# Kernel optimization log

Hardware: AMD Instinct MI355X
Metric: run time of the kernel (lower is better)

The kernel has to match this reference:

```python
import jax, jax.numpy as jnp
import numpy as np
import math

D_K = 1024
HEADS = 16
HEAD_DIM = 64

def setup_inputs() -> dict:
    key = jax.random.key(0)
    ks = jax.random.split(key, 9)
    B, S, E = 2, 2048, D_K
    sc = 0.02
    return {
        "x": jax.random.normal(ks[0], (B, S, E), dtype=jnp.float32),
        "mask": 1,
        "Wq": jax.random.normal(ks[1], (E, E), dtype=jnp.float32) * sc,
        "bq": jnp.zeros((E,), dtype=jnp.float32),
        "Wk": jax.random.normal(ks[2], (E, E), dtype=jnp.float32) * sc,
        "bk": jnp.zeros((E,), dtype=jnp.float32),
        "Wv": jax.random.normal(ks[3], (E, E), dtype=jnp.float32) * sc,
        "bv": jnp.zeros((E,), dtype=jnp.float32),
        "Wo": jax.random.normal(ks[4], (E, E), dtype=jnp.float32) * sc,
        "bo": jnp.zeros((E,), dtype=jnp.float32),
    }

def reference(x, mask, Wq, bq, Wk, bk, Wv, bv, Wo, bo):
    B, S, E = x.shape
    H, Dh = HEADS, HEAD_DIM
    # QKV projections; split heads: [B, H, S, Dh]
    q = (x @ Wq + bq).reshape(B, S, H, Dh).transpose(0, 2, 1, 3)
    k = (x @ Wk + bk).reshape(B, S, H, Dh).transpose(0, 2, 1, 3)
    v = (x @ Wv + bv).reshape(B, S, H, Dh).transpose(0, 2, 1, 3)
    # NOTE: original scales by sqrt(d_k) (full model dim), not sqrt(head_dim)
    scores = jnp.einsum('bhsd,bhtd->bhst', q, k) / math.sqrt(E)
    if mask:
        causal = jnp.tril(jnp.ones((S, S), dtype=bool))
        scores = jnp.where(causal[None, None], scores, jnp.float32(-1e9))
    attn = jax.nn.softmax(scores, axis=-1)
    out = jnp.einsum('bhst,bhtd->bhsd', attn, v)  # [B,H,S,Dh]
    out = out.transpose(0, 2, 1, 3).reshape(B, S, E)
    return out @ Wo + bo
```

## Files before the change

### kernel.cpp

```cpp
#include <hip/hip_runtime.h>

#define HEADS  16
#define DH     64
#define SEQ    2048
#define NBATCH 2
#define EMB    1024
#define MTOT   (NBATCH * SEQ)

#define QSCALE 0.045084220027780106f

typedef short  s16x8 __attribute__((ext_vector_type(8)));
typedef float  f32x4 __attribute__((ext_vector_type(4)));
typedef unsigned short u16;
typedef unsigned short u16x4 __attribute__((ext_vector_type(4)));

__device__ __forceinline__ u16 f2bf(float f) {
  unsigned u = __builtin_bit_cast(unsigned, f);
  u += 0x7fffu + ((u >> 16) & 1u);
  return (u16)(u >> 16);
}

__device__ __forceinline__ void gll16(const u16* g, u16* l) {
  __builtin_amdgcn_global_load_lds(
      (const __attribute__((address_space(1))) unsigned int*)g,
      (__attribute__((address_space(3))) unsigned int*)l, 16, 0, 0);
}

__global__ void cvt_x_kernel(const float* __restrict__ x, u16* __restrict__ xb) {
  int i = (blockIdx.x * 256 + threadIdx.x) * 4;
  float4 v = *(const float4*)(x + i);
  u16x4 o;
  o.x = f2bf(v.x); o.y = f2bf(v.y); o.z = f2bf(v.z); o.w = f2bf(v.w);
  *(u16x4*)(xb + i) = o;
}

__global__ void cvt_wt_kernel(const float* __restrict__ Wq, const float* __restrict__ Wk,
                              const float* __restrict__ Wv, const float* __restrict__ Wo,
                              u16* __restrict__ Wqt, u16* __restrict__ Wkt,
                              u16* __restrict__ Wvt, u16* __restrict__ Wot) {
  __shared__ float tile[32][33];
  const float* W; u16* T;
  switch (blockIdx.z) {
    case 0:  W = Wq; T = Wqt; break;
    case 1:  W = Wk; T = Wkt; break;
    case 2:  W = Wv; T = Wvt; break;
    default: W = Wo; T = Wot; break;
  }
  int n0 = blockIdx.x * 32, k0 = blockIdx.y * 32;
  int tx = threadIdx.x, ty = threadIdx.y;
#pragma unroll
  for (int r = 0; r < 32; r += 8)
    tile[ty + r][tx] = W[(size_t)(k0 + ty + r) * EMB + n0 + tx];
  __syncthreads();
#pragma unroll
  for (int r = 0; r < 32; r += 8)
    T[(size_t)(n0 + ty + r) * EMB + k0 + tx] = f2bf(tile[tx][ty + r]);
}

__global__ __launch_bounds__(512, 2) void gemm_qkv(const u16* __restrict__ xb,
                                                   const u16* __restrict__ Wqt, const u16* __restrict__ Wkt,
                                                   const u16* __restrict__ Wvt,
                                                   const float* __restrict__ bq, const float* __restrict__ bk,
                                                   const float* __restrict__ bv,
                                                   u16* __restrict__ Qb, u16* __restrict__ Kb,
                                                   u16* __restrict__ Vtb) {
  __shared__ __align__(16) u16 As[2][256 * 64];
  __shared__ __align__(16) u16 Bs[2][256 * 64];
  const int tid = threadIdx.x;
  const int lane = tid & 63, w = tid >> 6;
  const int wm = w >> 2, wn = w & 3;
  const int lr = lane & 15, lq = lane >> 4;

  const int lin  = blockIdx.x;
  const int job  = (lin & 7) * 24 + (lin >> 3);
  const int mode = job >> 6;
  const int rem  = job & 63;
  const int m0 = (rem >> 2) * 256, n0 = (rem & 3) * 256;

  const u16* Bt; const float* bias; u16* out;
  switch (mode) {
    case 0:  Bt = Wqt; bias = bq; out = Qb;  break;
    case 1:  Bt = Wkt; bias = bk; out = Kb;  break;
    default: Bt = Wvt; bias = bv; out = Vtb; break;
  }

  f32x4 acc[8][4];
#pragma unroll
  for (int i = 0; i < 8; i++)
#pragma unroll
    for (int j = 0; j < 4; j++)
      acc[i][j] = (f32x4){0.f, 0.f, 0.f, 0.f};

  auto stage = [&](int kt, int bi) {
    const int k0 = kt * 64;
#pragma unroll
    for (int j = 0; j < 4; j++) {
      int c = tid + 512 * j;
      int row = c >> 3, c8 = (c & 7) ^ (row & 7);
      gll16(&xb[(size_t)(m0 + row) * EMB + k0 + c8 * 8],
            &As[bi][(w * 64 + 512 * j) * 8]);
    }
#pragma unroll
    for (int j = 0; j < 4; j++) {
      int c = tid + 512 * j;
      int row = c >> 3, c8 = (c & 7) ^ (row & 7);
      gll16(&Bt[(size_t)(n0 + row) * EMB + k0 + c8 * 8],
            &Bs[bi][(w * 64 + 512 * j) * 8]);
    }
  };

  stage(0, 0);
  stage(1, 1);

  for (int kt = 0; kt < 16; ++kt) {
    const int bi = kt & 1;
    if (kt < 15) asm volatile("s_waitcnt vmcnt(8)" ::: "memory");
    else         asm volatile("s_waitcnt vmcnt(0)" ::: "memory");
    __builtin_amdgcn_s_barrier();

    const u16* Asc = As[bi];
    const u16* Bsc = Bs[bi];
#pragma unroll
    for (int kk8 = 0; kk8 < 8; kk8 += 4) {
      s16x8 bf[4];
#pragma unroll
      for (int j = 0; j < 4; j++) {
        int row = wn * 64 + j * 16 + lr;
        bf[j] = *(const s16x8*)&Bsc[row * 64 + (((kk8 + lq) ^ (row & 7)) * 8)];
      }
#pragma unroll
      for (int mh = 0; mh < 2; mh++) {
        s16x8 af[4];
#pragma unroll
        for (int i = 0; i < 4; i++) {
          int row = wm * 128 + mh * 64 + i * 16 + lr;
          af[i] = *(const s16x8*)&Asc[row * 64 + (((kk8 + lq) ^ (row & 7)) * 8)];
        }
        __builtin_amdgcn_s_setprio(1);
#pragma unroll
        for (int i = 0; i < 4; i++)
#pragma unroll
          for (int j = 0; j < 4; j++)
            acc[mh * 4 + i][j] =
                __builtin_amdgcn_mfma_f32_16x16x32_bf16(af[i], bf[j], acc[mh * 4 + i][j], 0, 0, 0);
        __builtin_amdgcn_s_setprio(0);
      }
    }

    asm volatile("s_waitcnt lgkmcnt(0)" ::: "memory");
    __builtin_amdgcn_s_barrier();
    __builtin_amdgcn_sched_barrier(0);
    if (kt + 2 < 16) stage(kt + 2, bi);
  }

#pragma unroll
  for (int mh = 0; mh < 2; mh++) {
#pragma unroll
    for (int i = 0; i < 4; i++) {
#pragma unroll
      for (int j = 0; j < 4; j++) {
        int col   = n0 + wn * 64 + j * 16 + lr;
        int mbase = m0 + wm * 128 + mh * 64 + i * 16 + lq * 4;
        float bv_ = bias[col];
        int h = col >> 6, d = col & 63;
        f32x4 a = acc[mh * 4 + i][j];
        if (mode == 0) {
#pragma unroll
          for (int r = 0; r < 4; r++) {
            int m = mbase + r, b = m >> 11, s = m & (SEQ - 1);
            out[((size_t)(b * HEADS + h) * SEQ + s) * DH + d] = f2bf((a[r] + bv_) * QSCALE);
          }
        } else if (mode == 1) {
#pragma unroll
          for (int r = 0; r < 4; r++) {
            int m = mbase + r, b = m >> 11, s = m & (SEQ - 1);
            out[((size_t)(b * HEADS + h) * SEQ + s) * DH + d] = f2bf(a[r] + bv_);
          }
        } else {
          int b = mbase >> 11, s = mbase & (SEQ - 1);
          u16x4 pk;
          pk.x = f2bf(a[0] + bv_);
          pk.y = f2bf(a[1] + bv_);
          pk.z = f2bf(a[2] + bv_);
          pk.w = f2bf(a[3] + bv_);
          *(u16x4*)&out[((size_t)(b * HEADS + h) * DH + d) * SEQ + s] = pk;
        }
      }
    }
  }
}

__device__ __forceinline__ void gemm_core64(const u16* __restrict__ A, const u16* __restrict__ Bt,
                                            u16* As, u16* Bs, int m0, int n0, f32x4 acc[4][2]) {
  const int tid = threadIdx.x;
  const int lane = tid & 63, w = tid >> 6;
  const int wm = w >> 1, wn = w & 1;
  const int lr = lane & 15, lq = lane >> 4;
#pragma unroll
  for (int i = 0; i < 4; i++)
#pragma unroll
    for (int j = 0; j < 2; j++)
      acc[i][j] = (f32x4){0.f, 0.f, 0.f, 0.f};

  for (int k0 = 0; k0 < EMB; k0 += 64) {
    __syncthreads();
#pragma unroll
    for (int j = 0; j < 4; j++) {
      int c = tid + 256 * j;
      int row = c >> 3, c8 = (c & 7) ^ (row & 7);
      gll16(&A[(size_t)(m0 + row) * EMB + k0 + c8 * 8],
            &As[(w * 64 + 256 * j) * 8]);
    }
#pragma unroll
    for (int j = 0; j < 2; j++) {
      int c = tid + 256 * j;
      int row = c >> 3, c8 = (c & 7) ^ (row & 7);
      gll16(&Bt[(size_t)(n0 + row) * EMB + k0 + c8 * 8],
            &Bs[(w * 64 + 256 * j) * 8]);
    }
    __syncthreads();
#pragma unroll
    for (int kk8 = 0; kk8 < 8; kk8 += 4) {
      s16x8 af[4], bf[2];
#pragma unroll
      for (int i = 0; i < 4; i++) {
        int row = wm * 64 + i * 16 + lr;
        af[i] = *(const s16x8*)&As[row * 64 + (((kk8 + lq) ^ (row & 7)) * 8)];
      }
#pragma unroll
      for (int j = 0; j < 2; j++) {
        int row = wn * 32 + j * 16 + lr;
        bf[j] = *(const s16x8*)&Bs[row * 64 + (((kk8 + lq) ^ (row & 7)) * 8)];
      }
#pragma unroll
      for (int i = 0; i < 4; i++)
#pragma unroll
        for (int j = 0; j < 2; j++)
          acc[i][j] = __builtin_amdgcn_mfma_f32_16x16x32_bf16(af[i], bf[j], acc[i][j], 0, 0, 0);
    }
  }
}

__global__ __launch_bounds__(256) void gemm_out(const u16* __restrict__ A, const u16* __restrict__ Bt,
                                                const float* __restrict__ bias, float* __restrict__ out) {
  __shared__ __align__(16) u16 As[128 * 64];
  __shared__ __align__(16) u16 Bs[64 * 64];
  const int lin = blockIdx.x + 16 * blockIdx.y;
  const int job = (lin & 7) * 64 + (lin >> 3);
  const int m0 = (job >> 4) * 128, n0 = (job & 15) * 64;
  f32x4 acc[4][2];
  gemm_core64(A, Bt, As, Bs, m0, n0, acc);

  const int tid = threadIdx.x, lane = tid & 63, w = tid >> 6;
  const int wm = w >> 1, wn = w & 1;
  const int lr = lane & 15, lq = lane >> 4;
#pragma unroll
  for (int i = 0; i < 4; i++) {
#pragma unroll
    for (int j = 0; j < 2; j++) {
      int col   = n0 + wn * 32 + j * 16 + lr;
      int mbase = m0 + wm * 64 + i * 16 + lq * 4;
      float bv_ = bias[col];
#pragma unroll
      for (int r = 0; r < 4; r++)
        out[(size_t)(mbase + r) * EMB + col] = acc[i][j][r] + bv_;
    }
  }
}

__global__ __launch_bounds__(512, 4) void attn_fwd(const u16* __restrict__ Q,
                                                   const u16* __restrict__ Kg,
                                                   const u16* __restrict__ Vt,
                                                   u16* __restrict__ O) {
  __shared__ __align__(16) u16 smem[33280];
  const int tid = threadIdx.x, lane = tid & 63, w = tid >> 6;
  const int g = w >> 2, wg = w & 3;
  const int lr = lane & 15, lq = lane >> 4;
  const int lin = blockIdx.x + 16 * blockIdx.y;
  const int job = (lin & 7) * 64 + (lin >> 3);
  const int bx = job & 15, bh = job >> 4;
  const int qtA = bx, qtB = 31 - bx;
  const int rowoff = wg * 16;
  u16* Ks = smem + (g ? 11520 : 0);
  u16* Vs = smem + (g ? 16640 : 5120);
  u16* pw = smem + 23040 + w * 1280;
  const size_t qkbase = (size_t)bh * SEQ * DH;
  const size_t vbase  = (size_t)bh * DH * SEQ;
  const u16* kgp = Kg + qkbase;
  const u16* vtp = Vt + vbase;
  const int t256 = tid & 255;
  const int b = bh >> 4, hh = bh & 15;

  {
    int r = t256 >> 4, c = (t256 & 15) * 4;
    u16 one = 0x3F80;
    u16x4 val = (r == 0) ? (u16x4){one, one, one, one} : (u16x4){0, 0, 0, 0};
    *(u16x4*)&Vs[(64 + r) * 80 + c] = val;
  }

  s16x8 qf0, qf1;
  {
    const int myqt0 = g ? qtB : qtA;
    const u16* qp = Q + qkbase + (size_t)(myqt0 * 64 + rowoff + lr) * DH;
    qf0 = *(const s16x8*)&qp[lq * 8];
    qf1 = *(const s16x8*)&qp[32 + lq * 8];
  }
  f32x4 o[4], os;
#pragma unroll
  for (int t = 0; t < 4; t++) o[t] = (f32x4){0.f, 0.f, 0.f, 0.f};
  os = (f32x4){0.f, 0.f, 0.f, 0.f};

  const int srow = t256 >> 3, soff = (t256 & 7) * 8;
  int kt0 = g ? (16 - bx) : 0;
  s16x8 kr0 = *(const s16x8*)&kgp[(size_t)(kt0 * 64 + srow) * DH + soff];
  s16x8 kr1 = *(const s16x8*)&kgp[(size_t)(kt0 * 64 + srow + 32) * DH + soff];
  s16x8 vr0 = *(const s16x8*)&vtp[(size_t)srow * SEQ + kt0 * 64 + soff];
  s16x8 vr1 = *(const s16x8*)&vtp[(size_t)(srow + 32) * SEQ + kt0 * 64 + soff];

  for (int i = 0; i < 17; ++i) {
    __syncthreads();
    *(s16x8*)&Ks[srow * 80 + soff]        = kr0;
    *(s16x8*)&Ks[(srow + 32) * 80 + soff] = kr1;
    *(s16x8*)&Vs[srow * 80 + soff]        = vr0;
    *(s16x8*)&Vs[(srow + 32) * 80 + soff] = vr1;
    __syncthreads();

    {
      bool hn = g ? (i + 1 < 16) : (i + 1 < 17);
      if (hn) {
        int ktn = g ? (17 + i - bx) : ((i + 1 <= qtA) ? (i + 1) : (i - qtA));
        kr0 = *(const s16x8*)&kgp[(size_t)(ktn * 64 + srow) * DH + soff];
        kr1 = *(const s16x8*)&kgp[(size_t)(ktn * 64 + srow + 32) * DH + soff];
        vr0 = *(const s16x8*)&vtp[(size_t)srow * SEQ + ktn * 64 + soff];
        vr1 = *(const s16x8*)&vtp[(size_t)(srow + 32) * SEQ + ktn * 64 + soff];
      }
    }

    if (g == 0 && i == qtA + 1) {
      float inv[4];
#pragma unroll
      for (int r = 0; r < 4; r++) inv[r] = __builtin_amdgcn_rcpf(__shfl(os[r], lq * 16));
#pragma unroll
      for (int t = 0; t < 4; t++)
#pragma unroll
        for (int r = 0; r < 4; r++) {
          int m = b * SEQ + qtA * 64 + rowoff + lq * 4 + r;
          O[(size_t)m * EMB + hh * 64 + t * 16 + lr] = f2bf(o[t][r] * inv[r]);
        }
#pragma unroll
      for (int t = 0; t < 4; t++) o[t] = (f32x4){0.f, 0.f, 0.f, 0.f};
      os = (f32x4){0.f, 0.f, 0.f, 0.f};
      const u16* qp = Q + qkbase + (size_t)(qtB * 64 + rowoff + lr) * DH;
      qf0 = *(const s16x8*)&qp[lq * 8];
      qf1 = *(const s16x8*)&qp[32 + lq * 8];
    }

    const bool docomp = g ? (i < 16) : true;
    if (docomp) {
      f32x4 sc[4];
      __builtin_amdgcn_s_setprio(1);
#pragma unroll
      for (int t = 0; t < 4; t++) {
        s16x8 kf0 = *(const s16x8*)&Ks[(t * 16 + lr) * 80 + lq * 8];
        s16x8 kf1 = *(const s16x8*)&Ks[(t * 16 + lr) * 80 + 32 + lq * 8];
        f32x4 z = (f32x4){0.f, 0.f, 0.f, 0.f};
        z = __builtin_amdgcn_mfma_f32_16x16x32_bf16(qf0, kf0, z, 0, 0, 0);
        z = __builtin_amdgcn_mfma_f32_16x16x32_bf16(qf1, kf1, z, 0, 0, 0);
        sc[t] = z;
      }
      __builtin_amdgcn_s_setprio(0);
      const bool diag = g ? (i == 15) : (i == qtA);
      if (diag) {
#pragma unroll
        for (int t = 0; t < 4; t++)
#pragma unroll
          for (int r = 0; r < 4; r++)
            if ((t * 16 + lr) > (rowoff + lq * 4 + r)) sc[t][r] = -1e9f;
      }
#pragma unroll
      for (int t = 0; t < 4; t++)
#pragma unroll
        for (int r = 0; r < 4; r++)
          sc[t][r] = __builtin_amdgcn_exp2f(sc[t][r]);

#pragma unroll
      for (int t = 0; t < 4; t++)
#pragma unroll
        for (int r = 0; r < 4; r++)
          pw[(lq * 4 + r) * 80 + t * 16 + lr] = f2bf(sc[t][r]);

      __builtin_amdgcn_s_setprio(1);
#pragma unroll
      for (int kc = 0; kc < 2; kc++) {
        s16x8 pf = *(const s16x8*)&pw[lr * 80 + kc * 32 + lq * 8];
#pragma unroll
        for (int t = 0; t < 4; t++) {
          s16x8 vf = *(const s16x8*)&Vs[(t * 16 + lr) * 80 + kc * 32 + lq * 8];
          o[t] = __builtin_amdgcn_mfma_f32_16x16x32_bf16(pf, vf, o[t], 0, 0, 0);
        }
        s16x8 sf = *(const s16x8*)&Vs[(64 + lr) * 80 + kc * 32 + lq * 8];
        os = __builtin_amdgcn_mfma_f32_16x16x32_bf16(pf, sf, os, 0, 0, 0);
      }
      __builtin_amdgcn_s_setprio(0);
    }
  }

  __syncthreads();
  float* Cb = (float*)smem;
  float* Ss = (float*)(smem + 23040);
  if (g == 0) {
#pragma unroll
    for (int t = 0; t < 4; t++)
#pragma unroll
      for (int r = 0; r < 4; r++)
        Cb[(rowoff + lq * 4 + r) * 68 + t * 16 + lr] = o[t][r];
#pragma unroll
    for (int r = 0; r < 4; r++) {
      float s = __shfl(os[r], lq * 16);
      if (lr == 0) Ss[rowoff + lq * 4 + r] = s;
    }
  }
  __syncthreads();
  if (g == 1) {
    float inv[4];
#pragma unroll
    for (int r = 0; r < 4; r++)
      inv[r] = __builtin_amdgcn_rcpf(__shfl(os[r], lq * 16) + Ss[rowoff + lq * 4 + r]);
#pragma unroll
    for (int t = 0; t < 4; t++)
#pragma unroll
      for (int r = 0; r < 4; r++) {
        int m = b * SEQ + qtB * 64 + rowoff + lq * 4 + r;
        float v = o[t][r] + Cb[(rowoff + lq * 4 + r) * 68 + t * 16 + lr];
        O[(size_t)m * EMB + hh * 64 + t * 16 + lr] = f2bf(v * inv[r]);
      }
  }
}

extern "C" void kernel_launch(void* const* d_in, const int* in_sizes, int n_in,
                              void* d_out, int out_size, void* d_ws, size_t ws_size,
                              hipStream_t stream) {
  const float* x  = (const float*)d_in[0];
  const float* Wq = (const float*)d_in[2];
  const float* bq = (const float*)d_in[3];
  const float* Wk = (const float*)d_in[4];
  const float* bk = (const float*)d_in[5];
  const float* Wv = (const float*)d_in[6];
  const float* bv = (const float*)d_in[7];
  const float* Wo = (const float*)d_in[8];
  const float* bo = (const float*)d_in[9];

  char* ws = (char*)d_ws;
  const size_t MB = 1024 * 1024;
  u16* Qb  = (u16*)(ws + 0 * MB);
  u16* Kb  = (u16*)(ws + 8 * MB);
  u16* Vtb = (u16*)(ws + 16 * MB);
  u16* xb  = (u16*)(ws + 24 * MB);
  u16* Ob  = xb;
  u16* Wqt = (u16*)(ws + 32 * MB);
  u16* Wkt = (u16*)(ws + 34 * MB);
  u16* Wvt = (u16*)(ws + 36 * MB);
  u16* Wot = (u16*)(ws + 38 * MB);

  cvt_x_kernel<<<(MTOT * EMB) / (256 * 4), 256, 0, stream>>>(x, xb);
  cvt_wt_kernel<<<dim3(EMB / 32, EMB / 32, 4), dim3(32, 8), 0, stream>>>(
      Wq, Wk, Wv, Wo, Wqt, Wkt, Wvt, Wot);

  gemm_qkv<<<dim3(192), 512, 0, stream>>>(
      xb, Wqt, Wkt, Wvt, bq, bk, bv, Qb, Kb, Vtb);

  attn_fwd<<<dim3(16, NBATCH * HEADS), 512, 0, stream>>>(Qb, Kb, Vtb, Ob);

  gemm_out<<<dim3(EMB / 64, MTOT / 128), 256, 0, stream>>>(Ob, Wot, bo, (float*)d_out);
}
```

Measured before the change: 186.7 us.

## Interleave global-to-LDS prefetch with MFMA phases in QKV projection GEMM

Restructures the QKV projection GEMM main loop from a two-stage-ahead prefetch into a four-phase ping-pong schedule. Each K-tile is split into four sub-steps that each load LDS fragments, issue a quarter of the next tile's global-to-LDS loads and run 16 MFMAs, separated by barriers. The goal is to spread memory traffic evenly across the compute and overlap it better. In exchange, prefetch depth drops to one tile, there are many more barriers per iteration, and a full vmcnt(0) wait at the end of each iteration can expose global load latency.

```diff
diff --git a/kernel.cpp b/kernel.cpp
--- a/kernel.cpp
+++ b/kernel.cpp
@@ -83,6 +83,8 @@
     case 1:  Bt = Wkt; bias = bk; out = Kb;  break;
     default: Bt = Wvt; bias = bv; out = Vtb; break;
   }
+  const u16* Ax = xb + (size_t)m0 * EMB;
+  const u16* Bx = Bt + (size_t)n0 * EMB;
 
   f32x4 acc[8][4];
 #pragma unroll
@@ -91,66 +93,84 @@
     for (int j = 0; j < 4; j++)
       acc[i][j] = (f32x4){0.f, 0.f, 0.f, 0.f};
 
-  auto stage = [&](int kt, int bi) {
-    const int k0 = kt * 64;
-#pragma unroll
-    for (int j = 0; j < 4; j++) {
+  auto stage2 = [&](const u16* src, u16* dst, int half, int k0) {
+#pragma unroll
+    for (int j = half * 2; j < half * 2 + 2; j++) {
       int c = tid + 512 * j;
       int row = c >> 3, c8 = (c & 7) ^ (row & 7);
-      gll16(&xb[(size_t)(m0 + row) * EMB + k0 + c8 * 8],
-            &As[bi][(w * 64 + 512 * j) * 8]);
-    }
+      gll16(&src[(size_t)row * EMB + k0 + c8 * 8], &dst[(w * 64 + 512 * j) * 8]);
+    }
+  };
+  auto ldsA = [&](const u16* buf, int kk8, int mh, s16x8 af[4]) {
+#pragma unroll
+    for (int i = 0; i < 4; i++) {
+      int row = wm * 128 + mh * 64 + i * 16 + lr;
+      af[i] = *(const s16x8*)&buf[row * 64 + (((kk8 + lq) ^ (row & 7)) * 8)];
+    }
+  };
+  auto ldsB = [&](const u16* buf, int kk8, s16x8 bf[4]) {
 #pragma unroll
     for (int j = 0; j < 4; j++) {
-      int c = tid + 512 * j;
-      int row = c >> 3, c8 = (c & 7) ^ (row & 7);
-      gll16(&Bt[(size_t)(n0 + row) * EMB + k0 + c8 * 8],
-            &Bs[bi][(w * 64 + 512 * j) * 8]);
+      int row = wn * 64 + j * 16 + lr;
+      bf[j] = *(const s16x8*)&buf[row * 64 + (((kk8 + lq) ^ (row & 7)) * 8)];
     }
   };
-
-  stage(0, 0);
-  stage(1, 1);
-
-  for (int kt = 0; kt < 16; ++kt) {
-    const int bi = kt & 1;
-    if (kt < 15) asm volatile("s_waitcnt vmcnt(8)" ::: "memory");
-    else         asm volatile("s_waitcnt vmcnt(0)" ::: "memory");
-    __builtin_amdgcn_s_barrier();
-
-    const u16* Asc = As[bi];
-    const u16* Bsc = Bs[bi];
-#pragma unroll
-    for (int kk8 = 0; kk8 < 8; kk8 += 4) {
-      s16x8 bf[4];
-#pragma unroll
-      for (int j = 0; j < 4; j++) {
-        int row = wn * 64 + j * 16 + lr;
-        bf[j] = *(const s16x8*)&Bsc[row * 64 + (((kk8 + lq) ^ (row & 7)) * 8)];
-      }
-#pragma unroll
-      for (int mh = 0; mh < 2; mh++) {
-        s16x8 af[4];
-#pragma unroll
-        for (int i = 0; i < 4; i++) {
-          int row = wm * 128 + mh * 64 + i * 16 + lr;
-          af[i] = *(const s16x8*)&Asc[row * 64 + (((kk8 + lq) ^ (row & 7)) * 8)];
-        }
-        __builtin_amdgcn_s_setprio(1);
-#pragma unroll
-        for (int i = 0; i < 4; i++)
-#pragma unroll
-          for (int j = 0; j < 4; j++)
-            acc[mh * 4 + i][j] =
-                __builtin_amdgcn_mfma_f32_16x16x32_bf16(af[i], bf[j], acc[mh * 4 + i][j], 0, 0, 0);
-        __builtin_amdgcn_s_setprio(0);
-      }
-    }
-
+  auto mma16 = [&](int mh, s16x8 af[4], s16x8 bf[4]) {
+    __builtin_amdgcn_s_setprio(1);
+#pragma unroll
+    for (int i = 0; i < 4; i++)
+#pragma unroll
+      for (int j = 0; j < 4; j++)
+        acc[mh * 4 + i][j] =
+            __builtin_amdgcn_mfma_f32_16x16x32_bf16(af[i], bf[j], acc[mh * 4 + i][j], 0, 0, 0);
+    __builtin_amdgcn_s_setprio(0);
+  };
+
+  stage2(Ax, As[0], 0, 0); stage2(Ax, As[0], 1, 0);
+  stage2(Bx, Bs[0], 0, 0); stage2(Bx, Bs[0], 1, 0);
+  asm volatile("s_waitcnt vmcnt(0)" ::: "memory");
+  __builtin_amdgcn_s_barrier();
+
+  for (int t = 0; t < 16; ++t) {
+    const int bi = t & 1, bn = bi ^ 1;
+    const int kn = (t + 1) * 64;
+    const bool st = (t < 15);
+    s16x8 af[4], bf[4];
+
+    ldsB(Bs[bi], 0, bf);
+    ldsA(As[bi], 0, 0, af);
+    if (st) stage2(Ax, As[bn], 0, kn);
+    __builtin_amdgcn_s_barrier();
     asm volatile("s_waitcnt lgkmcnt(0)" ::: "memory");
-    __builtin_amdgcn_s_barrier();
     __builtin_amdgcn_sched_barrier(0);
-    if (kt + 2 < 16) stage(kt + 2, bi);
+    mma16(0, af, bf);
+    __builtin_amdgcn_s_barrier();
+
+    ldsA(As[bi], 0, 1, af);
+    if (st) stage2(Ax, As[bn], 1, kn);
+    __builtin_amdgcn_s_barrier();
+    asm volatile("s_waitcnt lgkmcnt(0)" ::: "memory");
+    __builtin_amdgcn_sched_barrier(0);
+    mma16(1, af, bf);
+    __builtin_amdgcn_s_barrier();
+
+    ldsB(Bs[bi], 4, bf);
+    ldsA(As[bi], 4, 0, af);
+    if (st) stage2(Bx, Bs[bn], 0, kn);
+    __builtin_amdgcn_s_barrier();
+    asm volatile("s_waitcnt lgkmcnt(0)" ::: "memory");
+    __builtin_amdgcn_sched_barrier(0);
+    mma16(0, af, bf);
+    __builtin_amdgcn_s_barrier();
+
+    ldsA(As[bi], 4, 1, af);
+    if (st) stage2(Bx, Bs[bn], 1, kn);
+    __builtin_amdgcn_s_barrier();
+    asm volatile("s_waitcnt lgkmcnt(0)" ::: "memory");
+    __builtin_amdgcn_sched_barrier(0);
+    mma16(1, af, bf);
+    asm volatile("s_waitcnt vmcnt(0)" ::: "memory");
+    __builtin_amdgcn_s_barrier();
   }
 
 #pragma unroll
```

Result: no change. 189.0 us (+1.2%).
